# Kernel optimization log

Measured on AMD Instinct MI355X. Metric: run time of the kernel, lower is better.

## Reference

```python
import jax, jax.numpy as jnp
import numpy as np

N = 100_000      # nodes
E = 3_200_000    # edges
H = 32           # hidden_dim
L = 4            # num_layers
G = 1_000        # graphs in batch
F_IN = 1         # num_features
C = 2            # num_classes
BN_EPS = 1e-5


def setup_inputs() -> dict:
    key = jax.random.key(0)
    ks = jax.random.split(key, 8)
    s = 0.1  # param init scale
    x = jax.random.normal(ks[0], (N, F_IN), jnp.float32)
    edge_index = jax.random.randint(ks[1], (2, E), 0, N, dtype=jnp.int64)
    batch = jnp.sort(jax.random.randint(ks[2], (N,), 0, G, dtype=jnp.int64))
    return {
        "x": x,
        "edge_index": edge_index,
        "batch": batch,
        "W_enc": jax.random.normal(ks[3], (F_IN, H), jnp.float32) * s,
        "b_enc": jnp.zeros((H,), jnp.float32),
        "eps": jnp.zeros((L,), jnp.float32),           # GIN train_eps, init 0
        "W1": jax.random.normal(ks[4], (L, H, H), jnp.float32) * s,
        "b1": jnp.zeros((L, H), jnp.float32),
        "W2": jax.random.normal(ks[5], (L, H, H), jnp.float32) * s,
        "b2": jnp.zeros((L, H), jnp.float32),
        "gamma": jnp.ones((L, H), jnp.float32),
        "beta": jnp.zeros((L, H), jnp.float32),
        "W_cls": jax.random.normal(ks[6], (H, C), jnp.float32) * s,
        "b_cls": jnp.zeros((C,), jnp.float32),
    }


def reference(x, edge_index, batch, W_enc, b_enc, eps, W1, b1, W2, b2,
              gamma, beta, W_cls, b_cls):
    h = x @ W_enc + b_enc                      # [N, H] node encoder
    src, dst = edge_index[0], edge_index[1]    # message flow src -> dst
    for l in range(L):
        # GINConv: (1+eps)*x + sum_{j in N(i)} x_j
        agg = jax.ops.segment_sum(h[src], dst, num_segments=N)   # [N, H]
        z = (1.0 + eps[l]) * h + agg
        # 2-layer MLP
        z = jnp.maximum(z @ W1[l] + b1[l], 0.0) @ W2[l] + b2[l]
        # BatchNorm1d (training-mode batch statistics over nodes)
        mu = z.mean(axis=0)
        var = z.var(axis=0)
        z = gamma[l] * (z - mu) * jax.lax.rsqrt(var + BN_EPS) + beta[l]
        h = jnp.maximum(z, 0.0)                # ReLU (dropout = identity, eval)
    pooled = jax.ops.segment_sum(h, batch, num_segments=G)   # global_add_pool
    return pooled @ W_cls + b_cls              # [G, C]
```

## Files before the change

### kernel.cpp

```cpp
#include <hip/hip_runtime.h>

#define N_NODES 100000
#define N_EDGES 3200000
#define HD      32
#define NLAYERS 4
#define NGRAPHS 1000
#define BN_EPS  1e-5f
#define BSHIFT  9
#define NBUCK   ((N_NODES + 511) >> 9)
#define PCHUNK  8192
#define NPB     ((N_EDGES + PCHUNK - 1) / PCHUNK)
#define ZBLOCKS ((NGRAPHS * HD + 255) / 256)

typedef _Float16 f16;
typedef _Float16 f16x4 __attribute__((ext_vector_type(4)));
typedef _Float16 f16x8 __attribute__((ext_vector_type(8)));
typedef float    f32x4 __attribute__((ext_vector_type(4)));
typedef int      i32x4 __attribute__((ext_vector_type(4)));
typedef unsigned int  u32x2 __attribute__((ext_vector_type(2)));
typedef unsigned char uc8 __attribute__((ext_vector_type(8)));

__global__ __launch_bounds__(256) void k_encphist(
    const int* __restrict__ ei, float* __restrict__ stats,
    float* __restrict__ pooled, int* __restrict__ pcnt)
{
    __shared__ int hist[256];
    int bb = blockIdx.x, t = threadIdx.x;
    if (bb < NPB) {
        hist[t] = 0;
        __syncthreads();
        int base4 = bb * (PCHUNK / 4);
        int n4 = min(PCHUNK / 4, N_EDGES / 4 - base4);
        const i32x4* d4 = (const i32x4*)(ei + N_EDGES);
        for (int k = t; k < n4; k += 256) {
            i32x4 d = __builtin_nontemporal_load(d4 + base4 + k);
            atomicAdd(&hist[d.x >> BSHIFT], 1);
            atomicAdd(&hist[d.y >> BSHIFT], 1);
            atomicAdd(&hist[d.z >> BSHIFT], 1);
            atomicAdd(&hist[d.w >> BSHIFT], 1);
        }
        __syncthreads();
        pcnt[t * NPB + bb] = hist[t];
    } else {
        int gid = (bb - NPB) * 256 + t;
        if (gid < NLAYERS * 64)   stats[gid]  = 0.f;
        if (gid < NGRAPHS * HD)   pooled[gid] = 0.f;
    }
}

__global__ __launch_bounds__(512) void k_pscanA(int* __restrict__ pcnt,
                                                int* __restrict__ btot)
{
    __shared__ int sc[2][512];
    int t = threadIdx.x, b = blockIdx.x;
    int base = b * NPB;
    int v = (t < NPB) ? pcnt[base + t] : 0;
    int pp = 0;
    sc[0][t] = v;
    __syncthreads();
    for (int st = 1; st < 512; st <<= 1) {
        int x = sc[pp][t];
        if (t >= st) x += sc[pp][t - st];
        sc[pp ^ 1][t] = x;
        pp ^= 1;
        __syncthreads();
    }
    int incl = sc[pp][t];
    if (t < NPB) pcnt[base + t] = incl - v;
    if (t == NPB - 1) btot[b] = incl;
}

__global__ __launch_bounds__(256) void k_pscatter(const int* __restrict__ ei,
                                                  const int* __restrict__ pcnt,
                                                  const int* __restrict__ btot,
                                                  unsigned int* __restrict__ ebuf)
{
    __shared__ int sb[2][256];
    __shared__ int lcur[256];
    int t = threadIdx.x, blk = blockIdx.x;
    sb[0][t] = (t < NBUCK) ? btot[t] : 0;
    __syncthreads();
    int pp = 0;
    for (int st = 1; st < 256; st <<= 1) {
        int v = sb[pp][t];
        if (t >= st) v += sb[pp][t - st];
        sb[pp ^ 1][t] = v;
        pp ^= 1;
        __syncthreads();
    }
    int bexcl = (t == 0) ? 0 : sb[pp][t - 1];
    lcur[t] = pcnt[t * NPB + blk] + bexcl;
    __syncthreads();
    int base4 = blk * (PCHUNK / 4);
    int n4 = min(PCHUNK / 4, N_EDGES / 4 - base4);
    const i32x4* s4 = (const i32x4*)ei;
    const i32x4* d4 = (const i32x4*)(ei + N_EDGES);
    for (int k = t; k < n4; k += 256) {
        i32x4 s = __builtin_nontemporal_load(s4 + base4 + k);
        i32x4 d = __builtin_nontemporal_load(d4 + base4 + k);
        int pos;
        pos = atomicAdd(&lcur[d.x >> BSHIFT], 1);
        ebuf[pos] = ((unsigned)s.x << BSHIFT) | (unsigned)(d.x & 511);
        pos = atomicAdd(&lcur[d.y >> BSHIFT], 1);
        ebuf[pos] = ((unsigned)s.y << BSHIFT) | (unsigned)(d.y & 511);
        pos = atomicAdd(&lcur[d.z >> BSHIFT], 1);
        ebuf[pos] = ((unsigned)s.z << BSHIFT) | (unsigned)(d.z & 511);
        pos = atomicAdd(&lcur[d.w >> BSHIFT], 1);
        ebuf[pos] = ((unsigned)s.w << BSHIFT) | (unsigned)(d.w & 511);
    }
}

__global__ __launch_bounds__(512) void k_bfinal(const unsigned int* __restrict__ ebuf,
                                                const int* __restrict__ btot,
                                                const float* __restrict__ x,
                                                int* __restrict__ off,
                                                int* __restrict__ csr,
                                                float* __restrict__ usum)
{
    __shared__ int sb[2][256];
    __shared__ int cnt[512], scanbuf[2][512], cur[512];
    __shared__ float fsum[512];
    int tid = threadIdx.x, b = blockIdx.x;
    if (tid < 256) sb[0][tid] = (tid < NBUCK) ? btot[tid] : 0;
    fsum[tid] = 0.f;
    __syncthreads();
    int pp = 0;
    for (int st = 1; st < 256; st <<= 1) {
        if (tid < 256) {
            int v = sb[pp][tid];
            if (tid >= st) v += sb[pp][tid - st];
            sb[pp ^ 1][tid] = v;
        }
        pp ^= 1;
        __syncthreads();
    }
    int base = (b == 0) ? 0 : sb[pp][b - 1];
    int nE = sb[pp][b] - base;
    if (b == NBUCK - 1 && tid == 0) off[N_NODES] = sb[pp][NBUCK - 1];
    cnt[tid] = 0;
    __syncthreads();
    for (int e = tid; e < nE; e += 512)
        atomicAdd(&cnt[ebuf[base + e] & 511], 1);
    __syncthreads();
    int p2 = 0;
    scanbuf[0][tid] = cnt[tid];
    __syncthreads();
    for (int st = 1; st < 512; st <<= 1) {
        int v = scanbuf[p2][tid];
        if (tid >= st) v += scanbuf[p2][tid - st];
        scanbuf[p2 ^ 1][tid] = v;
        p2 ^= 1;
        __syncthreads();
    }
    int excl = scanbuf[p2][tid] - cnt[tid];
    cur[tid] = excl;
    int gnode = (b << BSHIFT) + tid;
    if (gnode < N_NODES) off[gnode] = base + excl;
    __syncthreads();
    for (int e = tid; e < nE; e += 512) {
        unsigned int p = ebuf[base + e];
        int src = (int)(p >> BSHIFT);
        int pos = atomicAdd(&cur[p & 511], 1);
        csr[base + pos] = src;
        atomicAdd(&fsum[p & 511], x[src]);
    }
    __syncthreads();
    if (gnode < N_NODES) usum[gnode] = fsum[tid];
}

__global__ __launch_bounds__(512, 8) void k_fused(
    const unsigned char* __restrict__ hq, const float* __restrict__ x,
    const float* __restrict__ usum, const int* __restrict__ off,
    const int* __restrict__ csr, const float* __restrict__ epsArr,
    const float* __restrict__ gamma, const float* __restrict__ beta,
    const float* __restrict__ W_enc, const float* __restrict__ b_enc,
    const float* __restrict__ W1, const float* __restrict__ b1,
    const float* __restrict__ W2, const float* __restrict__ b2,
    f16* __restrict__ z2out, float* __restrict__ stats, int layer)
{
    __shared__ f16 AT[64][40];
    __shared__ float T[4][16 * 36];
    __shared__ float redS[4][32], redQ[4][32];
    int tid = threadIdx.x, wave = tid >> 6, lane = tid & 63;
    int unit = tid >> 3, li = tid & 7;
    int lbase = lane & 56;
    int node = blockIdx.x * 64 + unit;
    int c0 = li * 4;

    if (node < N_NODES) {
        f16x4 r;
        if (layer == 0) {
            float oneEps = 1.f + epsArr[0];
            float u  = fmaf(oneEps, x[node], usum[node]);
            float dv = oneEps + (float)(off[node + 1] - off[node]);
            #pragma unroll
            for (int k = 0; k < 4; ++k)
                r[k] = (f16)(fmaf(u, W_enc[c0 + k], dv * b_enc[c0 + k]));
        } else {
            const unsigned MASK = 0x00FF00FFu;
            const unsigned char* hql = hq + c0;
            int j = off[node], jend = off[node + 1];
            int navail = jend - j;
            unsigned qv = *(const unsigned*)(hql + (size_t)node * 32);
            int ci0 = 0, ci1 = 0;
            if (li < navail)     ci0 = __builtin_nontemporal_load(csr + j + li);
            if (8 + li < navail) ci1 = __builtin_nontemporal_load(csr + j + 8 + li);
            unsigned a0 = 0, a1 = 0;
            while (navail >= 16) {
                unsigned g[16];
                #pragma unroll
                for (int e = 0; e < 8; ++e) {
                    int i0 = __shfl(ci0, lbase | e);
                    int i1 = __shfl(ci1, lbase | e);
                    g[e]     = *(const unsigned*)(hql + (size_t)i0 * 32);
                    g[e + 8] = *(const unsigned*)(hql + (size_t)i1 * 32);
                }
                j += 16; navail -= 16;
                if (li < navail)     ci0 = __builtin_nontemporal_load(csr + j + li);
                if (8 + li < navail) ci1 = __builtin_nontemporal_load(csr + j + 8 + li);
                #pragma unroll
                for (int e = 0; e < 16; ++e) {
                    a0 += g[e] & MASK; a1 += (g[e] >> 8) & MASK;
                }
            }
            if (navail >= 8) {
                unsigned g[8];
                #pragma unroll
                for (int e = 0; e < 8; ++e) {
                    int i0 = __shfl(ci0, lbase | e);
                    g[e] = *(const unsigned*)(hql + (size_t)i0 * 32);
                }
                ci0 = ci1; j += 8; navail -= 8;
                #pragma unroll
                for (int e = 0; e < 8; ++e) {
                    a0 += g[e] & MASK; a1 += (g[e] >> 8) & MASK;
                }
            }
            for (int e = 0; e < navail; ++e) {
                int i0 = __shfl(ci0, lbase | e);
                unsigned g = *(const unsigned*)(hql + (size_t)i0 * 32);
                a0 += g & MASK; a1 += (g >> 8) & MASK;
            }
            float oneEps = 1.f + epsArr[layer];
            float F[4];
            F[0] = (float)(a0 & 0xFFFF); F[2] = (float)(a0 >> 16);
            F[1] = (float)(a1 & 0xFFFF); F[3] = (float)(a1 >> 16);
            #pragma unroll
            for (int k = 0; k < 4; ++k) {
                float g  = gamma[(layer - 1) * 32 + c0 + k];
                float bb = beta[(layer - 1) * 32 + c0 + k];
                float s  = fmaxf(fmaxf(bb + 5.5f * fabsf(g), 0.f), 1e-6f) / 255.f;
                float q  = (float)((qv >> (8 * k)) & 255u);
                r[k] = (f16)(s * (F[k] + oneEps * q));
            }
        }
        *(f16x4*)&AT[unit][c0] = r;
    }
    __syncthreads();

    int col = lane & 15, quad = lane >> 4;
    float sA = 0.f, qA = 0.f, sB = 0.f, qB = 0.f;
    int nb = blockIdx.x * 64 + wave * 16;
    if (wave < 4 && nb < N_NODES) {
        f16x8 a = *(const f16x8*)&AT[wave * 16 + col][quad * 8];
        const float* W1l = W1 + layer * 1024;
        const float* W2l = W2 + layer * 1024;
        f16x8 w1a, w1b, w2a, w2b;
        #pragma unroll
        for (int jj = 0; jj < 8; ++jj) {
            int k = quad * 8 + jj;
            w1a[jj] = (f16)W1l[k * 32 + col];
            w1b[jj] = (f16)W1l[k * 32 + col + 16];
            w2a[jj] = (f16)W2l[k * 32 + col];
            w2b[jj] = (f16)W2l[k * 32 + col + 16];
        }
        float b1a = b1[layer * 32 + col], b1b = b1[layer * 32 + col + 16];
        float b2a = b2[layer * 32 + col], b2b = b2[layer * 32 + col + 16];
        f32x4 bias1a = {b1a, b1a, b1a, b1a}, bias1b = {b1b, b1b, b1b, b1b};
        f32x4 bias2a = {b2a, b2a, b2a, b2a}, bias2b = {b2b, b2b, b2b, b2b};
        float* Tw = T[wave];

        f32x4 m0 = __builtin_amdgcn_mfma_f32_16x16x32_f16(a, w1a, bias1a, 0, 0, 0);
        f32x4 m1 = __builtin_amdgcn_mfma_f32_16x16x32_f16(a, w1b, bias1b, 0, 0, 0);
        #pragma unroll
        for (int rr = 0; rr < 4; ++rr) {
            int row = quad * 4 + rr;
            Tw[row * 36 + col]      = fmaxf(m0[rr], 0.f);
            Tw[row * 36 + col + 16] = fmaxf(m1[rr], 0.f);
        }
        f32x4 t0 = *(const f32x4*)(Tw + col * 36 + quad * 8);
        f32x4 t1 = *(const f32x4*)(Tw + col * 36 + quad * 8 + 4);
        f16x8 a2;
        #pragma unroll
        for (int k = 0; k < 4; ++k) { a2[k] = (f16)t0[k]; a2[k + 4] = (f16)t1[k]; }
        f32x4 z0 = __builtin_amdgcn_mfma_f32_16x16x32_f16(a2, w2a, bias2a, 0, 0, 0);
        f32x4 zb = __builtin_amdgcn_mfma_f32_16x16x32_f16(a2, w2b, bias2b, 0, 0, 0);
        #pragma unroll
        for (int rr = 0; rr < 4; ++rr) {
            int n2 = nb + quad * 4 + rr;
            __builtin_nontemporal_store((f16)z0[rr], z2out + n2 * 32 + col);
            __builtin_nontemporal_store((f16)zb[rr], z2out + n2 * 32 + col + 16);
            sA += z0[rr]; qA += z0[rr] * z0[rr];
            sB += zb[rr]; qB += zb[rr] * zb[rr];
        }
    }
    if (wave < 4) {
        sA += __shfl_xor(sA, 16); sA += __shfl_xor(sA, 32);
        qA += __shfl_xor(qA, 16); qA += __shfl_xor(qA, 32);
        sB += __shfl_xor(sB, 16); sB += __shfl_xor(sB, 32);
        qB += __shfl_xor(qB, 16); qB += __shfl_xor(qB, 32);
        if (lane < 16) {
            redS[wave][col] = sA; redS[wave][col + 16] = sB;
            redQ[wave][col] = qA; redQ[wave][col + 16] = qB;
        }
    }
    __syncthreads();
    if (tid < 64) {
        int sel = tid >> 5, cc = tid & 31;
        float s = 0.f;
        #pragma unroll
        for (int w = 0; w < 4; ++w) s += sel ? redQ[w][cc] : redS[w][cc];
        atomicAdd(&stats[layer * 64 + sel * 32 + cc], s);
    }
}

__global__ __launch_bounds__(256) void k_quant(
    const f16* __restrict__ z2, const float* __restrict__ stats,
    const float* __restrict__ gamma, const float* __restrict__ beta,
    unsigned char* __restrict__ hq, int layer)
{
    int idx = blockIdx.x * 256 + threadIdx.x;
    if (idx >= N_NODES * 4) return;
    int c0 = (idx & 3) * 8;
    const float invN = 1.0f / (float)N_NODES;
    float bnsc[8], bnsh[8], inv_s[8];
    #pragma unroll
    for (int k = 0; k < 8; ++k) {
        int ch = c0 + k;
        float g = gamma[layer * 32 + ch], bb = beta[layer * 32 + ch];
        float mu  = stats[layer * 64 + ch] * invN;
        float var = stats[layer * 64 + 32 + ch] * invN - mu * mu;
        float sc = g * rsqrtf(var + BN_EPS);
        bnsc[k] = sc;
        bnsh[k] = bb - mu * sc;
        float vmax = fmaxf(bb + 5.5f * fabsf(g), 0.f);
        inv_s[k] = 255.f / fmaxf(vmax, 1e-6f);
    }
    f16x8 z = *(const f16x8*)(z2 + (size_t)idx * 8);
    uc8 r;
    #pragma unroll
    for (int k = 0; k < 8; ++k) {
        float v = fmaxf(fmaf((float)z[k], bnsc[k], bnsh[k]), 0.f);
        int q = (int)(fminf(v * inv_s[k], 255.f) + 0.5f);
        r[k] = (unsigned char)q;
    }
    __builtin_nontemporal_store(r, (uc8*)(hq + (size_t)idx * 8));
}

__global__ __launch_bounds__(256) void k_pool(const f16* __restrict__ z2,
                                              const int* __restrict__ batch,
                                              const float* __restrict__ stats,
                                              const float* __restrict__ gamma,
                                              const float* __restrict__ beta,
                                              float* __restrict__ pooled)
{
    int c = threadIdx.x & 31, slot = threadIdx.x >> 5;
    const float invN = 1.0f / (float)N_NODES;
    float mu  = stats[3 * 64 + c] * invN;
    float var = stats[3 * 64 + 32 + c] * invN - mu * mu;
    float sc = gamma[3 * 32 + c] * rsqrtf(var + BN_EPS);
    float sh = beta[3 * 32 + c] - mu * sc;
    int start = blockIdx.x * 256 + slot * 32;
    if (start >= N_NODES) return;
    int end = min(start + 32, N_NODES);
    int cur = batch[start]; float acc = 0.f;
    for (int i = start; i < end; ++i) {
        int g = batch[i];
        if (g != cur) { atomicAdd(&pooled[cur * HD + c], acc); acc = 0.f; cur = g; }
        acc += fmaxf(fmaf((float)z2[i * 32 + c], sc, sh), 0.f);
    }
    atomicAdd(&pooled[cur * HD + c], acc);
}

__global__ __launch_bounds__(256) void k_cls(const float* __restrict__ pooled,
                                             const float* __restrict__ Wc,
                                             const float* __restrict__ bc,
                                             float* __restrict__ out)
{
    int gid = blockIdx.x * 256 + threadIdx.x;
    if (gid >= NGRAPHS * 2) return;
    int g = gid >> 1, c = gid & 1;
    float s = bc[c];
    #pragma unroll
    for (int k = 0; k < 32; ++k) s = fmaf(pooled[g * 32 + k], Wc[k * 2 + c], s);
    out[gid] = s;
}

extern "C" void kernel_launch(void* const* d_in, const int* in_sizes, int n_in,
                              void* d_out, int out_size, void* d_ws, size_t ws_size,
                              hipStream_t stream)
{
    const float* x      = (const float*)d_in[0];
    const int*   ei     = (const int*)d_in[1];
    const int*   batch  = (const int*)d_in[2];
    const float* W_enc  = (const float*)d_in[3];
    const float* b_enc  = (const float*)d_in[4];
    const float* epsArr = (const float*)d_in[5];
    const float* W1     = (const float*)d_in[6];
    const float* b1     = (const float*)d_in[7];
    const float* W2     = (const float*)d_in[8];
    const float* b2     = (const float*)d_in[9];
    const float* gamma  = (const float*)d_in[10];
    const float* beta   = (const float*)d_in[11];
    const float* Wc     = (const float*)d_in[12];
    const float* bc     = (const float*)d_in[13];
    float* out = (float*)d_out;

    char* ws = (char*)d_ws;
    size_t o = 0;
    auto alloc = [&](size_t bytes) {
        char* p = ws + o;
        o += (bytes + 255) & ~(size_t)255;
        return p;
    };
    unsigned char* hq = (unsigned char*)alloc((size_t)N_NODES * 32);
    f16*   z2     = (f16*) alloc((size_t)N_NODES * 32 * 2);
    int*   csr    = (int*) alloc((size_t)N_EDGES * 4);
    unsigned int* ebuf = (unsigned int*)alloc((size_t)N_EDGES * 4);
    int*   offA   = (int*) alloc((size_t)(N_NODES + 1) * 4);
    float* usum   = (float*)alloc((size_t)N_NODES * 4);
    int*   pcnt   = (int*) alloc((size_t)256 * NPB * 4);
    int*   btot   = (int*) alloc(1024);
    float* stats  = (float*)alloc(NLAYERS * 64 * 4);
    float* pooled = (float*)alloc((size_t)NGRAPHS * HD * 4);

    k_encphist<<<NPB + ZBLOCKS, 256, 0, stream>>>(ei, stats, pooled, pcnt);
    k_pscanA  <<<NBUCK, 512, 0, stream>>>(pcnt, btot);
    k_pscatter<<<NPB, 256, 0, stream>>>(ei, pcnt, btot, ebuf);
    k_bfinal  <<<NBUCK, 512, 0, stream>>>(ebuf, btot, x, offA, csr, usum);

    for (int l = 0; l < NLAYERS; ++l) {
        k_fused<<<(N_NODES + 63) / 64, 512, 0, stream>>>(
            hq, x, usum, offA, csr, epsArr, gamma, beta, W_enc, b_enc,
            W1, b1, W2, b2, z2, stats, l);
        if (l < NLAYERS - 1)
            k_quant<<<(N_NODES * 4 + 255) / 256, 256, 0, stream>>>(z2, stats,
                                                                   gamma, beta,
                                                                   hq, l);
    }
    k_pool<<<(N_NODES + 255) / 256, 256, 0, stream>>>(z2, batch, stats,
                                                      gamma, beta, pooled);
    k_cls <<<8, 256, 0, stream>>>(pooled, Wc, bc, out);
}
```

Baseline: 419.1 us.

## Move layer-0 scalar neighbour sum into fused kernel and use L2-scoped gather loads

Drops the shared-memory float atomic accumulation of x[src] from the CSR build kernel and instead computes the layer-0 neighbour sum inside the fused layer kernel by walking the CSR with 8 lanes per node and a shuffle reduction. Neighbour gathers of the quantized features and of x now use relaxed agent-scope atomic loads, so they are served from L2 rather than polluting or missing in L1. Index math switches to 32-bit shifts, and nontemporal stores of z2 and hq become plain stores so the data stays cache-resident for the next kernel. The layer-0 kernel now does an extra gather pass over all edges, in exchange for removing the usum buffer and the LDS float atomics.

```diff
diff --git a/kernel.cpp b/kernel.cpp
--- a/kernel.cpp
+++ b/kernel.cpp
@@ -19,6 +19,11 @@
 typedef int      i32x4 __attribute__((ext_vector_type(4)));
 typedef unsigned int  u32x2 __attribute__((ext_vector_type(2)));
 typedef unsigned char uc8 __attribute__((ext_vector_type(8)));
+
+__device__ __forceinline__ unsigned ld_l2_u32(const void* p) {
+    return __hip_atomic_load((const unsigned*)p, __ATOMIC_RELAXED,
+                             __HIP_MEMORY_SCOPE_AGENT);
+}
 
 __global__ __launch_bounds__(256) void k_encphist(
     const int* __restrict__ ei, float* __restrict__ stats,
@@ -112,17 +117,13 @@
 
 __global__ __launch_bounds__(512) void k_bfinal(const unsigned int* __restrict__ ebuf,
                                                 const int* __restrict__ btot,
-                                                const float* __restrict__ x,
                                                 int* __restrict__ off,
-                                                int* __restrict__ csr,
-                                                float* __restrict__ usum)
+                                                int* __restrict__ csr)
 {
     __shared__ int sb[2][256];
     __shared__ int cnt[512], scanbuf[2][512], cur[512];
-    __shared__ float fsum[512];
     int tid = threadIdx.x, b = blockIdx.x;
     if (tid < 256) sb[0][tid] = (tid < NBUCK) ? btot[tid] : 0;
-    fsum[tid] = 0.f;
     __syncthreads();
     int pp = 0;
     for (int st = 1; st < 256; st <<= 1) {
@@ -159,24 +160,20 @@
     __syncthreads();
     for (int e = tid; e < nE; e += 512) {
         unsigned int p = ebuf[base + e];
-        int src = (int)(p >> BSHIFT);
         int pos = atomicAdd(&cur[p & 511], 1);
-        csr[base + pos] = src;
-        atomicAdd(&fsum[p & 511], x[src]);
-    }
-    __syncthreads();
-    if (gnode < N_NODES) usum[gnode] = fsum[tid];
+        csr[base + pos] = (int)(p >> BSHIFT);
+    }
 }
 
 __global__ __launch_bounds__(512, 8) void k_fused(
     const unsigned char* __restrict__ hq, const float* __restrict__ x,
-    const float* __restrict__ usum, const int* __restrict__ off,
-    const int* __restrict__ csr, const float* __restrict__ epsArr,
-    const float* __restrict__ gamma, const float* __restrict__ beta,
-    const float* __restrict__ W_enc, const float* __restrict__ b_enc,
-    const float* __restrict__ W1, const float* __restrict__ b1,
-    const float* __restrict__ W2, const float* __restrict__ b2,
-    f16* __restrict__ z2out, float* __restrict__ stats, int layer)
+    const int* __restrict__ off, const int* __restrict__ csr,
+    const float* __restrict__ epsArr, const float* __restrict__ gamma,
+    const float* __restrict__ beta, const float* __restrict__ W_enc,
+    const float* __restrict__ b_enc, const float* __restrict__ W1,
+    const float* __restrict__ b1, const float* __restrict__ W2,
+    const float* __restrict__ b2, f16* __restrict__ z2out,
+    float* __restrict__ stats, int layer)
 {
     __shared__ f16 AT[64][40];
     __shared__ float T[4][16 * 36];
@@ -190,9 +187,27 @@
     if (node < N_NODES) {
         f16x4 r;
         if (layer == 0) {
+            int j0 = off[node], jend = off[node + 1];
+            float S = 0.f;
+            int jj = j0 + li;
+            while (jj + 8 < jend) {
+                int i0 = __builtin_nontemporal_load(csr + jj);
+                int i1 = __builtin_nontemporal_load(csr + jj + 8);
+                unsigned xa = ld_l2_u32(x + i0);
+                unsigned xb = ld_l2_u32(x + i1);
+                S += __uint_as_float(xa) + __uint_as_float(xb);
+                jj += 16;
+            }
+            if (jj < jend) {
+                int i0 = __builtin_nontemporal_load(csr + jj);
+                S += __uint_as_float(ld_l2_u32(x + i0));
+            }
+            S += __shfl_xor(S, 1);
+            S += __shfl_xor(S, 2);
+            S += __shfl_xor(S, 4);
             float oneEps = 1.f + epsArr[0];
-            float u  = fmaf(oneEps, x[node], usum[node]);
-            float dv = oneEps + (float)(off[node + 1] - off[node]);
+            float u  = fmaf(oneEps, x[node], S);
+            float dv = oneEps + (float)(jend - j0);
             #pragma unroll
             for (int k = 0; k < 4; ++k)
                 r[k] = (f16)(fmaf(u, W_enc[c0 + k], dv * b_enc[c0 + k]));
@@ -201,7 +216,7 @@
             const unsigned char* hql = hq + c0;
             int j = off[node], jend = off[node + 1];
             int navail = jend - j;
-            unsigned qv = *(const unsigned*)(hql + (size_t)node * 32);
+            unsigned qv = *(const unsigned*)(hql + ((unsigned)node << 5));
             int ci0 = 0, ci1 = 0;
             if (li < navail)     ci0 = __builtin_nontemporal_load(csr + j + li);
             if (8 + li < navail) ci1 = __builtin_nontemporal_load(csr + j + 8 + li);
@@ -212,8 +227,8 @@
                 for (int e = 0; e < 8; ++e) {
                     int i0 = __shfl(ci0, lbase | e);
                     int i1 = __shfl(ci1, lbase | e);
-                    g[e]     = *(const unsigned*)(hql + (size_t)i0 * 32);
-                    g[e + 8] = *(const unsigned*)(hql + (size_t)i1 * 32);
+                    g[e]     = ld_l2_u32(hql + ((unsigned)i0 << 5));
+                    g[e + 8] = ld_l2_u32(hql + ((unsigned)i1 << 5));
                 }
                 j += 16; navail -= 16;
                 if (li < navail)     ci0 = __builtin_nontemporal_load(csr + j + li);
@@ -228,7 +243,7 @@
                 #pragma unroll
                 for (int e = 0; e < 8; ++e) {
                     int i0 = __shfl(ci0, lbase | e);
-                    g[e] = *(const unsigned*)(hql + (size_t)i0 * 32);
+                    g[e] = ld_l2_u32(hql + ((unsigned)i0 << 5));
                 }
                 ci0 = ci1; j += 8; navail -= 8;
                 #pragma unroll
@@ -238,7 +253,7 @@
             }
             for (int e = 0; e < navail; ++e) {
                 int i0 = __shfl(ci0, lbase | e);
-                unsigned g = *(const unsigned*)(hql + (size_t)i0 * 32);
+                unsigned g = ld_l2_u32(hql + ((unsigned)i0 << 5));
                 a0 += g & MASK; a1 += (g >> 8) & MASK;
             }
             float oneEps = 1.f + epsArr[layer];
@@ -298,8 +313,8 @@
         #pragma unroll
         for (int rr = 0; rr < 4; ++rr) {
             int n2 = nb + quad * 4 + rr;
-            __builtin_nontemporal_store((f16)z0[rr], z2out + n2 * 32 + col);
-            __builtin_nontemporal_store((f16)zb[rr], z2out + n2 * 32 + col + 16);
+            z2out[n2 * 32 + col]      = (f16)z0[rr];
+            z2out[n2 * 32 + col + 16] = (f16)zb[rr];
             sA += z0[rr]; qA += z0[rr] * z0[rr];
             sB += zb[rr]; qB += zb[rr] * zb[rr];
         }
@@ -354,7 +369,7 @@
         int q = (int)(fminf(v * inv_s[k], 255.f) + 0.5f);
         r[k] = (unsigned char)q;
     }
-    __builtin_nontemporal_store(r, (uc8*)(hq + (size_t)idx * 8));
+    *(uc8*)(hq + (size_t)idx * 8) = r;
 }
 
 __global__ __launch_bounds__(256) void k_pool(const f16* __restrict__ z2,
@@ -428,7 +443,6 @@
     int*   csr    = (int*) alloc((size_t)N_EDGES * 4);
     unsigned int* ebuf = (unsigned int*)alloc((size_t)N_EDGES * 4);
     int*   offA   = (int*) alloc((size_t)(N_NODES + 1) * 4);
-    float* usum   = (float*)alloc((size_t)N_NODES * 4);
     int*   pcnt   = (int*) alloc((size_t)256 * NPB * 4);
     int*   btot   = (int*) alloc(1024);
     float* stats  = (float*)alloc(NLAYERS * 64 * 4);
@@ -437,11 +451,11 @@
     k_encphist<<<NPB + ZBLOCKS, 256, 0, stream>>>(ei, stats, pooled, pcnt);
     k_pscanA  <<<NBUCK, 512, 0, stream>>>(pcnt, btot);
     k_pscatter<<<NPB, 256, 0, stream>>>(ei, pcnt, btot, ebuf);
-    k_bfinal  <<<NBUCK, 512, 0, stream>>>(ebuf, btot, x, offA, csr, usum);
+    k_bfinal  <<<NBUCK, 512, 0, stream>>>(ebuf, btot, offA, csr);
 
     for (int l = 0; l < NLAYERS; ++l) {
         k_fused<<<(N_NODES + 63) / 64, 512, 0, stream>>>(
-            hq, x, usum, offA, csr, epsArr, gamma, beta, W_enc, b_enc,
+            hq, x, offA, csr, epsArr, gamma, beta, W_enc, b_enc,
             W1, b1, W2, b2, z2, stats, l);
         if (l < NLAYERS - 1)
             k_quant<<<(N_NODES * 4 + 255) / 256, 256, 0, stream>>>(z2, stats,
```

After: 416.6 us. No clear change (-0.6%).
